# Kernel optimization log

Measured on AMD Instinct MI355X. Metric: run time of the kernel, lower is better.

## Reference

```python
import jax, jax.numpy as jnp
import numpy as np
from jax import lax

B, T, I, H, O = 4096, 512, 10, 32, 1

def setup_inputs() -> dict:
    key = jax.random.key(0)
    ks = jax.random.split(key, 7)
    s = 1.0 / np.sqrt(H)
    return {
        "x": jax.random.normal(ks[0], (B, T, I), dtype=jnp.float32),
        "W_ih": jax.random.uniform(ks[1], (4 * H, I), minval=-s, maxval=s, dtype=jnp.float32),
        "W_hh": jax.random.uniform(ks[2], (4 * H, H), minval=-s, maxval=s, dtype=jnp.float32),
        "b_ih": jax.random.uniform(ks[3], (4 * H,), minval=-s, maxval=s, dtype=jnp.float32),
        "b_hh": jax.random.uniform(ks[4], (4 * H,), minval=-s, maxval=s, dtype=jnp.float32),
        "W_dense": jax.random.uniform(ks[5], (O, H), minval=-s, maxval=s, dtype=jnp.float32),
        "b_dense": jax.random.uniform(ks[6], (O,), minval=-s, maxval=s, dtype=jnp.float32),
    }

def reference(x, W_ih, W_hh, b_ih, b_hh, W_dense, b_dense):
    # x: [B, T, I]; PyTorch LSTM gate order: i, f, g, o.
    b, t, _ = x.shape
    h = W_hh.shape[1]
    # Precompute input contribution for all timesteps: [T, B, 4H]
    gates_x = jnp.einsum('bti,gi->tbg', x, W_ih) + b_ih + b_hh

    def step(carry, gx):
        h_prev, c_prev = carry
        g = gx + h_prev @ W_hh.T  # [B, 4H]
        i_g = jax.nn.sigmoid(g[:, 0 * h:1 * h])
        f_g = jax.nn.sigmoid(g[:, 1 * h:2 * h])
        g_g = jnp.tanh(g[:, 2 * h:3 * h])
        o_g = jax.nn.sigmoid(g[:, 3 * h:4 * h])
        c = f_g * c_prev + i_g * g_g
        h_new = o_g * jnp.tanh(c)
        return (h_new, c), None

    init = (jnp.zeros((b, h), x.dtype), jnp.zeros((b, h), x.dtype))
    (h_last, _), _ = lax.scan(step, init, gates_x)
    # dropout in eval mode = identity
    return h_last @ W_dense.T + b_dense
```

## Files before the change

### kernel.cpp

```cpp
#include <hip/hip_runtime.h>


#define T_SZ 512
#define I_SZ 10
#define H_SZ 32

typedef _Float16 half8  __attribute__((ext_vector_type(8)));
typedef __fp16   fp16x2 __attribute__((ext_vector_type(2)));
typedef float    f32x4  __attribute__((ext_vector_type(4)));
typedef int      i32x4  __attribute__((ext_vector_type(4)));

union FH { i32x4 i; half8 h; };
static __device__ __forceinline__ half8 fragv(i32x4 v) { FH u; u.i = v; return u.h; }
static __device__ __forceinline__ half8 frag4(int a, int b, int c, int d) {
    FH u; u.i = (i32x4){a, b, c, d}; return u.h;
}

static __device__ __forceinline__ int pk16(float lo, float hi) {
    union { fp16x2 h; int i; } u;
    u.h = __builtin_amdgcn_cvt_pkrtz(lo, hi);
    return u.i;
}

#define MFMAH(A, B, C) __builtin_amdgcn_mfma_f32_16x16x32_f16((A), (B), (C), 0, 0, 0)
#define EXP2(x) __builtin_amdgcn_exp2f(x)
#define RCP(x)  __builtin_amdgcn_rcpf(x)

__global__ __launch_bounds__(64, 2)
void lstm_wave(const float* __restrict__ x, const float* __restrict__ W_ih,
               const float* __restrict__ W_hh, const float* __restrict__ b_ih,
               const float* __restrict__ b_hh, const float* __restrict__ W_dense,
               const float* __restrict__ b_dense, float* __restrict__ out)
{
    const int lane  = threadIdx.x;
    const int L     = lane & 15;
    const int Q     = lane >> 4;
    const int bbase = blockIdx.x * 2;

    const int bA   = L >> 3;
    const int bAct = Q >> 1;
    const int hidA = L + 16 * (Q & 1);

    int bhh[8][4];
    int bm[8][4];
    #pragma unroll
    for (int tau = 0; tau < 8; ++tau) {
        const int wr = 32 * (tau >> 1) + 16 * (tau & 1) + L;
        const float* ph = W_hh + wr * H_SZ + 8 * Q;
        #pragma unroll
        for (int d = 0; d < 4; ++d) {
            float2 v = *(const float2*)(ph + 2 * d);
            bhh[tau][d] = pk16(v.x, v.y);
        }
        if (Q == 0) {
            const float* pi = W_ih + wr * I_SZ;
            #pragma unroll
            for (int d = 0; d < 4; ++d) {
                float2 v = *(const float2*)(pi + 2 * d);
                bm[tau][d] = pk16(v.x, v.y);
            }
        } else if (Q == 1) {
            float2 v = *(const float2*)(W_ih + wr * I_SZ + 8);
            bm[tau][0] = pk16(v.x, v.y);
            #pragma unroll
            for (int d = 1; d < 4; ++d) {
                float2 w = *(const float2*)(W_hh + wr * H_SZ + 8 + 2 * d);
                bm[tau][d] = pk16(w.x, w.y);
            }
        } else {
            bm[tau][0] = bhh[tau][0]; bm[tau][1] = bhh[tau][1];
            bm[tau][2] = bhh[tau][2]; bm[tau][3] = bhh[tau][3];
        }
    }

    const float nL = -1.4426950f;
    const float m2 = -2.8853901f;
    const float mbi = nL * (b_ih[hidA]      + b_hh[hidA]);
    const float mbf = nL * (b_ih[32 + hidA] + b_hh[32 + hidA]);
    const float mbg = m2 * (b_ih[64 + hidA] + b_hh[64 + hidA]);
    const float mbo = nL * (b_ih[96 + hidA] + b_hh[96 + hidA]);

    __shared__ __attribute__((aligned(16))) _Float16 hbuf[2][2][2][H_SZ];
    {
        int* zz = (int*)&hbuf[0][0][0][0];
        zz[lane] = 0;
        zz[lane + 64] = 0;
    }

    const float* xrow = x + (size_t)(bbase + bA) * (T_SZ * I_SZ);
    float2 xa0 = *(const float2*)(xrow + 0), xa1 = *(const float2*)(xrow + 2),
           xa2 = *(const float2*)(xrow + 4), xa3 = *(const float2*)(xrow + 6),
           xa4 = *(const float2*)(xrow + 8);
    float2 xb0 = *(const float2*)(xrow + I_SZ + 0), xb1 = *(const float2*)(xrow + I_SZ + 2),
           xb2 = *(const float2*)(xrow + I_SZ + 4), xb3 = *(const float2*)(xrow + I_SZ + 6),
           xb4 = *(const float2*)(xrow + I_SZ + 8);

    const f32x4 zerov = {0.f, 0.f, 0.f, 0.f};
    float cst = 0.0f;
    float hlast = 0.0f;
    const bool q0 = (Q == 0), q1 = (Q == 1);
    const bool qh = (Q & 1);

    if ((blockIdx.x >> 10) & 1)
        __builtin_amdgcn_s_sleep(8);

    for (int t = 0; t < T_SZ; t += 2) {
        #pragma unroll
        for (int u = 0; u < 2; ++u) {
            const int rb = u, wb = u ^ 1;

            i32x4 hhi_ = *(const i32x4*)&hbuf[rb][0][bA][8 * Q];
            i32x4 lo_  = *(const i32x4*)&hbuf[rb][1][bA][8 * Q];

            float2 y0 = u ? xb0 : xa0, y1 = u ? xb1 : xa1, y2 = u ? xb2 : xa2,
                   y3 = u ? xb3 : xa3, y4 = u ? xb4 : xa4;
            int p0 = pk16(y0.x, y0.y), p1 = pk16(y1.x, y1.y), p2 = pk16(y2.x, y2.y),
                p3 = pk16(y3.x, y3.y), p4 = pk16(y4.x, y4.y);

            half8 mf = fragv((i32x4){ q0 ? p0 : (q1 ? p4 : lo_[0]),
                                      q0 ? p1 : lo_[1],
                                      q0 ? p2 : lo_[2],
                                      q0 ? p3 : lo_[3] });
            half8 hhi = fragv(hhi_);

            __builtin_amdgcn_s_setprio(1);
            f32x4 a0 = MFMAH(mf,  frag4(bm[0][0],  bm[0][1],  bm[0][2],  bm[0][3]),  zerov);
            a0       = MFMAH(hhi, frag4(bhh[0][0], bhh[0][1], bhh[0][2], bhh[0][3]), a0);
            f32x4 a1 = MFMAH(mf,  frag4(bm[1][0],  bm[1][1],  bm[1][2],  bm[1][3]),  zerov);
            a1       = MFMAH(hhi, frag4(bhh[1][0], bhh[1][1], bhh[1][2], bhh[1][3]), a1);
            float eA = EXP2(fmaf(nL, qh ? a1[0] : a0[0], mbi));

            f32x4 a2 = MFMAH(mf,  frag4(bm[2][0],  bm[2][1],  bm[2][2],  bm[2][3]),  zerov);
            a2       = MFMAH(hhi, frag4(bhh[2][0], bhh[2][1], bhh[2][2], bhh[2][3]), a2);
            f32x4 a3 = MFMAH(mf,  frag4(bm[3][0],  bm[3][1],  bm[3][2],  bm[3][3]),  zerov);
            a3       = MFMAH(hhi, frag4(bhh[3][0], bhh[3][1], bhh[3][2], bhh[3][3]), a3);
            float eF = EXP2(fmaf(nL, qh ? a3[0] : a2[0], mbf));

            f32x4 a4 = MFMAH(mf,  frag4(bm[4][0],  bm[4][1],  bm[4][2],  bm[4][3]),  zerov);
            a4       = MFMAH(hhi, frag4(bhh[4][0], bhh[4][1], bhh[4][2], bhh[4][3]), a4);
            f32x4 a5 = MFMAH(mf,  frag4(bm[5][0],  bm[5][1],  bm[5][2],  bm[5][3]),  zerov);
            a5       = MFMAH(hhi, frag4(bhh[5][0], bhh[5][1], bhh[5][2], bhh[5][3]), a5);
            float eG = EXP2(fmaf(m2, qh ? a5[0] : a4[0], mbg));

            f32x4 a6 = MFMAH(mf,  frag4(bm[6][0],  bm[6][1],  bm[6][2],  bm[6][3]),  zerov);
            a6       = MFMAH(hhi, frag4(bhh[6][0], bhh[6][1], bhh[6][2], bhh[6][3]), a6);
            f32x4 a7 = MFMAH(mf,  frag4(bm[7][0],  bm[7][1],  bm[7][2],  bm[7][3]),  zerov);
            a7       = MFMAH(hhi, frag4(bhh[7][0], bhh[7][1], bhh[7][2], bhh[7][3]), a7);
            __builtin_amdgcn_s_setprio(0);
            float eO = EXP2(fmaf(nL, qh ? a7[0] : a6[0], mbo));

            if (t + 2 + u < T_SZ) {
                const float* xr = xrow + (t + 2 + u) * I_SZ;
                if (u == 0) {
                    xa0 = *(const float2*)(xr + 0); xa1 = *(const float2*)(xr + 2);
                    xa2 = *(const float2*)(xr + 4); xa3 = *(const float2*)(xr + 6);
                    xa4 = *(const float2*)(xr + 8);
                } else {
                    xb0 = *(const float2*)(xr + 0); xb1 = *(const float2*)(xr + 2);
                    xb2 = *(const float2*)(xr + 4); xb3 = *(const float2*)(xr + 6);
                    xb4 = *(const float2*)(xr + 8);
                }
            }

            float fg  = RCP(1.0f + eF);
            float igg = (1.0f - eG) * RCP((1.0f + eA) * (1.0f + eG));
            cst = fmaf(fg, cst, igg);
            float eD = EXP2(m2 * cst);
            float hv = (1.0f - eD) * RCP((1.0f + eO) * (1.0f + eD));
            hlast = hv;

            _Float16 hh = (_Float16)hv;
            _Float16 hl = (_Float16)(hv - (float)hh);
            hbuf[wb][0][bAct][hidA] = hh;
            hbuf[wb][1][bAct][hidA] = hl;
        }
    }

    float v = hlast * W_dense[hidA];
    #pragma unroll
    for (int m = 16; m >= 1; m >>= 1)
        v += __shfl_xor(v, m);
    if (lane == 0)  out[bbase + 0] = v + b_dense[0];
    if (lane == 32) out[bbase + 1] = v + b_dense[0];
}

extern "C" void kernel_launch(void* const* d_in, const int* in_sizes, int n_in,
                              void* d_out, int out_size, void* d_ws, size_t ws_size,
                              hipStream_t stream) {
    const float* x       = (const float*)d_in[0];
    const float* W_ih    = (const float*)d_in[1];
    const float* W_hh    = (const float*)d_in[2];
    const float* b_ih    = (const float*)d_in[3];
    const float* b_hh    = (const float*)d_in[4];
    const float* W_dense = (const float*)d_in[5];
    const float* b_dense = (const float*)d_in[6];
    float* out = (float*)d_out;

    lstm_wave<<<dim3(2048), dim3(64), 0, stream>>>(
        x, W_ih, W_hh, b_ih, b_hh, W_dense, b_dense, out);
}
```

Before: 333.3 us.

## Split LSTM gate work across two waves per block with barrier-synced hidden exchange

```diff
diff --git a/kernel.cpp b/kernel.cpp
--- a/kernel.cpp
+++ b/kernel.cpp
@@ -26,66 +26,68 @@
 #define EXP2(x) __builtin_amdgcn_exp2f(x)
 #define RCP(x)  __builtin_amdgcn_rcpf(x)
 
-__global__ __launch_bounds__(64, 2)
+__global__ __launch_bounds__(128, 2)
 void lstm_wave(const float* __restrict__ x, const float* __restrict__ W_ih,
                const float* __restrict__ W_hh, const float* __restrict__ b_ih,
                const float* __restrict__ b_hh, const float* __restrict__ W_dense,
                const float* __restrict__ b_dense, float* __restrict__ out)
 {
-    const int lane  = threadIdx.x;
+    const int tid   = threadIdx.x;
+    const int lane  = tid & 63;
+    const int wid   = tid >> 6;
     const int L     = lane & 15;
     const int Q     = lane >> 4;
-    const int bbase = blockIdx.x * 2;
+    const int bbase = blockIdx.x * 4;
 
-    const int bA   = L >> 3;
-    const int bAct = Q >> 1;
-    const int hidA = L + 16 * (Q & 1);
+    const int bA  = L >> 2;
+    const int hid = L + 16 * wid;
 
-    int bhh[8][4];
-    int bm[8][4];
+    int bhh[4][4];
+    int bm[4][4];
     #pragma unroll
-    for (int tau = 0; tau < 8; ++tau) {
-        const int wr = 32 * (tau >> 1) + 16 * (tau & 1) + L;
+    for (int gt = 0; gt < 4; ++gt) {
+        const int wr = 32 * gt + 16 * wid + L;
         const float* ph = W_hh + wr * H_SZ + 8 * Q;
         #pragma unroll
         for (int d = 0; d < 4; ++d) {
             float2 v = *(const float2*)(ph + 2 * d);
-            bhh[tau][d] = pk16(v.x, v.y);
+            bhh[gt][d] = pk16(v.x, v.y);
         }
         if (Q == 0) {
             const float* pi = W_ih + wr * I_SZ;
             #pragma unroll
             for (int d = 0; d < 4; ++d) {
                 float2 v = *(const float2*)(pi + 2 * d);
-                bm[tau][d] = pk16(v.x, v.y);
+                bm[gt][d] = pk16(v.x, v.y);
             }
         } else if (Q == 1) {
             float2 v = *(const float2*)(W_ih + wr * I_SZ + 8);
-            bm[tau][0] = pk16(v.x, v.y);
+            bm[gt][0] = pk16(v.x, v.y);
             #pragma unroll
             for (int d = 1; d < 4; ++d) {
                 float2 w = *(const float2*)(W_hh + wr * H_SZ + 8 + 2 * d);
-                bm[tau][d] = pk16(w.x, w.y);
+                bm[gt][d] = pk16(w.x, w.y);
             }
         } else {
-            bm[tau][0] = bhh[tau][0]; bm[tau][1] = bhh[tau][1];
-            bm[tau][2] = bhh[tau][2]; bm[tau][3] = bhh[tau][3];
+            bm[gt][0] = bhh[gt][0]; bm[gt][1] = bhh[gt][1];
+            bm[gt][2] = bhh[gt][2]; bm[gt][3] = bhh[gt][3];
         }
     }
 
     const float nL = -1.4426950f;
     const float m2 = -2.8853901f;
-    const float mbi = nL * (b_ih[hidA]      + b_hh[hidA]);
-    const float mbf = nL * (b_ih[32 + hidA] + b_hh[32 + hidA]);
-    const float mbg = m2 * (b_ih[64 + hidA] + b_hh[64 + hidA]);
-    const float mbo = nL * (b_ih[96 + hidA] + b_hh[96 + hidA]);
+    const float mbi = nL * (b_ih[hid]      + b_hh[hid]);
+    const float mbf = nL * (b_ih[32 + hid] + b_hh[32 + hid]);
+    const float mbg = m2 * (b_ih[64 + hid] + b_hh[64 + hid]);
+    const float mbo = nL * (b_ih[96 + hid] + b_hh[96 + hid]);
 
-    __shared__ __attribute__((aligned(16))) _Float16 hbuf[2][2][2][H_SZ];
+    __shared__ __attribute__((aligned(16))) _Float16 hbuf[2][2][4][H_SZ];
+    __shared__ float redbuf[2][4];
     {
         int* zz = (int*)&hbuf[0][0][0][0];
-        zz[lane] = 0;
-        zz[lane + 64] = 0;
+        zz[tid] = 0; zz[tid + 128] = 0;
     }
+    __syncthreads();
 
     const float* xrow = x + (size_t)(bbase + bA) * (T_SZ * I_SZ);
     float2 xa0 = *(const float2*)(xrow + 0), xa1 = *(const float2*)(xrow + 2),
@@ -99,10 +101,6 @@
     float cst = 0.0f;
     float hlast = 0.0f;
     const bool q0 = (Q == 0), q1 = (Q == 1);
-    const bool qh = (Q & 1);
-
-    if ((blockIdx.x >> 10) & 1)
-        __builtin_amdgcn_s_sleep(8);
 
     for (int t = 0; t < T_SZ; t += 2) {
         #pragma unroll
@@ -123,32 +121,6 @@
                                       q0 ? p3 : lo_[3] });
             half8 hhi = fragv(hhi_);
 
-            __builtin_amdgcn_s_setprio(1);
-            f32x4 a0 = MFMAH(mf,  frag4(bm[0][0],  bm[0][1],  bm[0][2],  bm[0][3]),  zerov);
-            a0       = MFMAH(hhi, frag4(bhh[0][0], bhh[0][1], bhh[0][2], bhh[0][3]), a0);
-            f32x4 a1 = MFMAH(mf,  frag4(bm[1][0],  bm[1][1],  bm[1][2],  bm[1][3]),  zerov);
-            a1       = MFMAH(hhi, frag4(bhh[1][0], bhh[1][1], bhh[1][2], bhh[1][3]), a1);
-            float eA = EXP2(fmaf(nL, qh ? a1[0] : a0[0], mbi));
-
-            f32x4 a2 = MFMAH(mf,  frag4(bm[2][0],  bm[2][1],  bm[2][2],  bm[2][3]),  zerov);
-            a2       = MFMAH(hhi, frag4(bhh[2][0], bhh[2][1], bhh[2][2], bhh[2][3]), a2);
-            f32x4 a3 = MFMAH(mf,  frag4(bm[3][0],  bm[3][1],  bm[3][2],  bm[3][3]),  zerov);
-            a3       = MFMAH(hhi, frag4(bhh[3][0], bhh[3][1], bhh[3][2], bhh[3][3]), a3);
-            float eF = EXP2(fmaf(nL, qh ? a3[0] : a2[0], mbf));
-
-            f32x4 a4 = MFMAH(mf,  frag4(bm[4][0],  bm[4][1],  bm[4][2],  bm[4][3]),  zerov);
-            a4       = MFMAH(hhi, frag4(bhh[4][0], bhh[4][1], bhh[4][2], bhh[4][3]), a4);
-            f32x4 a5 = MFMAH(mf,  frag4(bm[5][0],  bm[5][1],  bm[5][2],  bm[5][3]),  zerov);
-            a5       = MFMAH(hhi, frag4(bhh[5][0], bhh[5][1], bhh[5][2], bhh[5][3]), a5);
-            float eG = EXP2(fmaf(m2, qh ? a5[0] : a4[0], mbg));
-
-            f32x4 a6 = MFMAH(mf,  frag4(bm[6][0],  bm[6][1],  bm[6][2],  bm[6][3]),  zerov);
-            a6       = MFMAH(hhi, frag4(bhh[6][0], bhh[6][1], bhh[6][2], bhh[6][3]), a6);
-            f32x4 a7 = MFMAH(mf,  frag4(bm[7][0],  bm[7][1],  bm[7][2],  bm[7][3]),  zerov);
-            a7       = MFMAH(hhi, frag4(bhh[7][0], bhh[7][1], bhh[7][2], bhh[7][3]), a7);
-            __builtin_amdgcn_s_setprio(0);
-            float eO = EXP2(fmaf(nL, qh ? a7[0] : a6[0], mbo));
-
             if (t + 2 + u < T_SZ) {
                 const float* xr = xrow + (t + 2 + u) * I_SZ;
                 if (u == 0) {
@@ -162,6 +134,19 @@
                 }
             }
 
+            f32x4 a0 = MFMAH(mf,  frag4(bm[0][0],  bm[0][1],  bm[0][2],  bm[0][3]),  zerov);
+            a0       = MFMAH(hhi, frag4(bhh[0][0], bhh[0][1], bhh[0][2], bhh[0][3]), a0);
+            f32x4 a1 = MFMAH(mf,  frag4(bm[1][0],  bm[1][1],  bm[1][2],  bm[1][3]),  zerov);
+            a1       = MFMAH(hhi, frag4(bhh[1][0], bhh[1][1], bhh[1][2], bhh[1][3]), a1);
+            float eA = EXP2(fmaf(nL, a0[0], mbi));
+            f32x4 a2 = MFMAH(mf,  frag4(bm[2][0],  bm[2][1],  bm[2][2],  bm[2][3]),  zerov);
+            a2       = MFMAH(hhi, frag4(bhh[2][0], bhh[2][1], bhh[2][2], bhh[2][3]), a2);
+            float eF = EXP2(fmaf(nL, a1[0], mbf));
+            f32x4 a3 = MFMAH(mf,  frag4(bm[3][0],  bm[3][1],  bm[3][2],  bm[3][3]),  zerov);
+            a3       = MFMAH(hhi, frag4(bhh[3][0], bhh[3][1], bhh[3][2], bhh[3][3]), a3);
+            float eG = EXP2(fmaf(m2, a2[0], mbg));
+            float eO = EXP2(fmaf(nL, a3[0], mbo));
+
             float fg  = RCP(1.0f + eF);
             float igg = (1.0f - eG) * RCP((1.0f + eA) * (1.0f + eG));
             cst = fmaf(fg, cst, igg);
@@ -171,17 +156,20 @@
 
             _Float16 hh = (_Float16)hv;
             _Float16 hl = (_Float16)(hv - (float)hh);
-            hbuf[wb][0][bAct][hidA] = hh;
-            hbuf[wb][1][bAct][hidA] = hl;
+            hbuf[wb][0][Q][hid] = hh;
+            hbuf[wb][1][Q][hid] = hl;
+
+            __syncthreads();
         }
     }
 
-    float v = hlast * W_dense[hidA];
+    float v = hlast * W_dense[hid];
     #pragma unroll
-    for (int m = 16; m >= 1; m >>= 1)
+    for (int m = 8; m >= 1; m >>= 1)
         v += __shfl_xor(v, m);
-    if (lane == 0)  out[bbase + 0] = v + b_dense[0];
-    if (lane == 32) out[bbase + 1] = v + b_dense[0];
+    if (L == 0) redbuf[wid][Q] = v;
+    __syncthreads();
+    if (tid < 4) out[bbase + tid] = redbuf[0][tid] + redbuf[1][tid] + b_dense[0];
 }
 
 extern "C" void kernel_launch(void* const* d_in, const int* in_sizes, int n_in,
@@ -196,6 +184,6 @@
     const float* b_dense = (const float*)d_in[6];
     float* out = (float*)d_out;
 
-    lstm_wave<<<dim3(2048), dim3(64), 0, stream>>>(
+    lstm_wave<<<dim3(1024), dim3(128), 0, stream>>>(
         x, W_ih, W_hh, b_ih, b_hh, W_dense, b_dense, out);
 }
```

After: 353.6 us. 1.06x slower.
